# Kernel optimization log

Measured on AMD Instinct MI355X. Metric: run time of the kernel, lower is better.

## Reference

```python
import jax, jax.numpy as jnp
import numpy as np

BS, L, H, HD, R, HID = 4, 2048, 12, 64, 16, 768


def setup_inputs() -> dict:
    key = jax.random.key(0)
    k0, k1, k2, k3 = jax.random.split(key, 4)
    xavier = np.sqrt(2.0 / (H + HD))  # xavier_normal_ on (H, HD)
    lin = 1.0 / np.sqrt(HID)
    return {
        "hidden_states": jax.random.normal(k0, (BS, L, HID), jnp.float32),
        "K1_w": jax.random.normal(k1, (HID, H * HD), jnp.float32) * lin,
        "K1_b": jnp.zeros((H * HD,), jnp.float32),
        "V1_w": jax.random.normal(k2, (HID, H * HD), jnp.float32) * lin,
        "V1_b": jnp.zeros((H * HD,), jnp.float32),
        "ReadingHead": jax.random.normal(k3, (H, HD), jnp.float32) * xavier,
        "bidirection_weight": jnp.full((1, 1, H, 1, 2 * R), 1.0 / (2 * R), jnp.float32),
    }


def _scan_mmap(valid_mask, reverse):
    # valid_mask: (bs, L, H) bool. Sequential register-shift scan over positions 1..L-1.
    bs, Ln, Hn = valid_mask.shape
    idxs = jnp.arange(1, Ln, dtype=jnp.int32)
    masks = jnp.swapaxes(valid_mask[:, 1:], 0, 1)  # (L-1, bs, H)
    if reverse:
        idxs = idxs[::-1]
        masks = masks[::-1]
    init = jnp.zeros((bs, R + 1, Hn), jnp.int32)

    def step(valids, xm):
        i, m = xm
        valids = valids.at[:, 0].set(i)  # slot 0 <- current index (matches in-place torch order)
        shifted = jnp.where(m[:, None, :], valids[:, :-1], valids[:, 1:])
        valids = valids.at[:, 1:].set(shifted)
        return valids, valids[:, 1:]

    _, out = jax.lax.scan(step, init, (idxs, masks))  # (L-1, bs, R, H)
    if reverse:
        out = out[::-1]
    out = jnp.concatenate([jnp.zeros((1, bs, R, Hn), jnp.int32), out], axis=0)
    return jnp.swapaxes(out, 0, 1)  # (bs, L, R, H)


def reference(hidden_states, K1_w, K1_b, V1_w, V1_b, ReadingHead, bidirection_weight):
    K1 = jax.nn.relu(hidden_states @ K1_w + K1_b).reshape(BS, L, H, HD)
    V1 = jax.nn.relu(hidden_states @ V1_w + V1_b).reshape(BS, L, H, HD)
    dot_products = jnp.einsum('blhn,hn->blh', K1, ReadingHead)
    valid_mask = dot_products > 0.5  # attn_var default branch
    fm = _scan_mmap(valid_mask, False).reshape(BS, L * R, H)
    bm = _scan_mmap(valid_mask, True).reshape(BS, L * R, H)
    V_forward = jnp.take_along_axis(V1, fm[..., None], axis=1).reshape(BS, L, R, H, HD)
    V_backward = jnp.take_along_axis(V1, bm[..., None], axis=1).reshape(BS, L, R, H, HD)
    w = bidirection_weight[0, 0, :, 0, :]  # (H, 2R); first R -> forward, last R -> backward
    ctx = (jnp.einsum('blrhd,hr->blhd', V_forward, w[:, :R])
           + jnp.einsum('blrhd,hr->blhd', V_backward, w[:, R:]))
    return ctx.reshape(BS, L, H * HD)
```

## Files before the change

### kernel.cpp

```cpp
#include <hip/hip_runtime.h>
#include <hip/hip_bf16.h>

#define BS 4
#define L 2048
#define H 12
#define HD 64
#define R 16
#define HID 768
#define MARGIN 0.02f
#define FIXCAP 16384
#define FIXGRID 1024

typedef __attribute__((ext_vector_type(8))) short s8v;
typedef __attribute__((ext_vector_type(4))) float f32x4;

typedef __attribute__((address_space(1))) const void as1_void;
typedef __attribute__((address_space(3))) void as3_void;
#define GLOAD_LDS16(g, l) \
    __builtin_amdgcn_global_load_lds((as1_void*)(g), (as3_void*)(l), 16, 0, 0)

static __device__ __forceinline__ unsigned short f2bf_bits(float f) {
    __hip_bfloat16 h = __float2bfloat16(f);
    return *reinterpret_cast<unsigned short*>(&h);
}

__global__ __launch_bounds__(256) void convert_hs(
    const float* __restrict__ in, __hip_bfloat16* __restrict__ out,
    int* __restrict__ fixcnt)
{
    if (blockIdx.x == 0 && threadIdx.x == 0) *fixcnt = 0;
    int i = (blockIdx.x * 256 + threadIdx.x) * 4;
    float4 v = *(const float4*)&in[i];
    ushort4 o;
    o.x = f2bf_bits(v.x); o.y = f2bf_bits(v.y);
    o.z = f2bf_bits(v.z); o.w = f2bf_bits(v.w);
    *(ushort4*)&out[i] = o;
}

__global__ __launch_bounds__(256) void transpose_wt2(
    const float* __restrict__ K1w, const float* __restrict__ V1w,
    __hip_bfloat16* __restrict__ WtK, __hip_bfloat16* __restrict__ WtV)
{
    const float* in = blockIdx.z ? V1w : K1w;
    __hip_bfloat16* out = blockIdx.z ? WtV : WtK;
    __shared__ float s[32][33];
    const int c = threadIdx.x & 31, r8 = threadIdx.x >> 5;
    const int kt = blockIdx.x * 32, nt = blockIdx.y * 32;
#pragma unroll
    for (int rr = 0; rr < 4; ++rr) {
        int k = r8 + rr * 8;
        s[k][c] = in[(size_t)(kt + k) * HID + nt + c];
    }
    __syncthreads();
#pragma unroll
    for (int rr = 0; rr < 4; ++rr) {
        int n = r8 + rr * 8;
        out[(size_t)(nt + n) * HID + kt + c] = __float2bfloat16(s[c][n]);
    }
}

__global__ __launch_bounds__(256) void gemm_fused(
    const __hip_bfloat16* __restrict__ A,
    const __hip_bfloat16* __restrict__ WtK,
    const __hip_bfloat16* __restrict__ WtV,
    const float* __restrict__ K1b,
    const float* __restrict__ V1b,
    const float* __restrict__ RH,
    float* __restrict__ dots,
    int* __restrict__ fixlist,
    int* __restrict__ fixcnt,
    __hip_bfloat16* __restrict__ C)
{
    __shared__ alignas(16) __hip_bfloat16 As[128 * 64];
    __shared__ alignas(16) __hip_bfloat16 Bs[128 * 64];

    const int tid = threadIdx.x;
    const bool isV = blockIdx.y < 6;
    const int m0 = blockIdx.x * 128;
    const int n0 = (isV ? blockIdx.y : blockIdx.y - 6) * 128;
    const __hip_bfloat16* Bt = isV ? WtV : WtK;

    const int wid = tid >> 6, lane = tid & 63;
    const int quad = lane >> 4, lm = lane & 15;
    const int wm = wid & 1, wn = wid >> 1;

    const int srow = lane >> 3;
    const int schk = (lane & 7) ^ ((lane >> 3) & 7);
    const __hip_bfloat16* gA =
        A + (size_t)(m0 + 32 * wid + srow) * HID + schk * 8;
    const __hip_bfloat16* gB =
        Bt + (size_t)(n0 + 32 * wid + srow) * HID + schk * 8;
    __hip_bfloat16* lA = &As[(32 * wid) * 64];
    __hip_bfloat16* lB = &Bs[(32 * wid) * 64];

    const int s7 = lm & 7;
    const __hip_bfloat16* pA0 = &As[(wm * 64 + lm) * 64 + ((quad ^ s7) * 8)];
    const __hip_bfloat16* pA1 = &As[(wm * 64 + lm) * 64 + (((4 + quad) ^ s7) * 8)];
    const __hip_bfloat16* pB0 = &Bs[(wn * 64 + lm) * 64 + ((quad ^ s7) * 8)];
    const __hip_bfloat16* pB1 = &Bs[(wn * 64 + lm) * 64 + (((4 + quad) ^ s7) * 8)];

    f32x4 acc[4][4] = {};

    for (int k0 = 0; k0 < HID; k0 += 64) {
#pragma unroll
        for (int d = 0; d < 4; ++d) {
            GLOAD_LDS16(gA + (size_t)(8 * d) * HID, lA + (8 * d) * 64);
            GLOAD_LDS16(gB + (size_t)(8 * d) * HID, lB + (8 * d) * 64);
        }
        gA += 64; gB += 64;
        __syncthreads();

        s8v af[4], bf[4];
#pragma unroll
        for (int i = 0; i < 4; ++i) af[i] = *(const s8v*)(pA0 + i * 16 * 64);
#pragma unroll
        for (int j = 0; j < 4; ++j) bf[j] = *(const s8v*)(pB0 + j * 16 * 64);
#pragma unroll
        for (int i = 0; i < 4; ++i)
#pragma unroll
            for (int j = 0; j < 4; ++j)
                acc[i][j] = __builtin_amdgcn_mfma_f32_16x16x32_bf16(
                    af[i], bf[j], acc[i][j], 0, 0, 0);
#pragma unroll
        for (int i = 0; i < 4; ++i) af[i] = *(const s8v*)(pA1 + i * 16 * 64);
#pragma unroll
        for (int j = 0; j < 4; ++j) bf[j] = *(const s8v*)(pB1 + j * 16 * 64);
#pragma unroll
        for (int i = 0; i < 4; ++i)
#pragma unroll
            for (int j = 0; j < 4; ++j)
                acc[i][j] = __builtin_amdgcn_mfma_f32_16x16x32_bf16(
                    af[i], bf[j], acc[i][j], 0, 0, 0);
        __syncthreads();
    }

    if (isV) {
#pragma unroll
        for (int i = 0; i < 4; ++i) {
            int row_b = m0 + wm * 64 + i * 16 + quad * 4;
#pragma unroll
            for (int j = 0; j < 4; ++j) {
                int col = n0 + wn * 64 + j * 16 + lm;
                float bsv = V1b[col];
#pragma unroll
                for (int reg = 0; reg < 4; ++reg) {
                    float v = acc[i][j][reg] + bsv;
                    C[(size_t)(row_b + reg) * HID + col] =
                        __float2bfloat16(fmaxf(v, 0.f));
                }
            }
        }
    } else {
        const int head = (n0 >> 6) + wn;
        float bj[4], rj[4];
#pragma unroll
        for (int j = 0; j < 4; ++j) {
            bj[j] = K1b[head * 64 + j * 16 + lm];
            rj[j] = RH[head * 64 + j * 16 + lm];
        }
#pragma unroll
        for (int i = 0; i < 4; ++i) {
            int row0 = m0 + wm * 64 + i * 16 + quad * 4;
#pragma unroll
            for (int reg = 0; reg < 4; ++reg) {
                float p = 0.f;
#pragma unroll
                for (int j = 0; j < 4; ++j)
                    p = fmaf(fmaxf(acc[i][j][reg] + bj[j], 0.f), rj[j], p);
                p += __shfl_xor(p, 1, 64);
                p += __shfl_xor(p, 2, 64);
                p += __shfl_xor(p, 4, 64);
                p += __shfl_xor(p, 8, 64);
                if (lm == 0) {
                    int row = row0 + reg;
                    int b = row >> 11, l = row & (L - 1);
                    dots[((b * H + head) << 11) + l] = p;
                    if (fabsf(p - 0.5f) < MARGIN) {
                        int idx = atomicAdd(fixcnt, 1);
                        if (idx < FIXCAP) fixlist[idx] = row * 16 + head;
                    }
                }
            }
        }
    }
}

__global__ __launch_bounds__(256) void fixup_kernel(
    const float* __restrict__ hs,
    const float* __restrict__ W,
    const float* __restrict__ bias,
    const float* __restrict__ RH,
    const int* __restrict__ fixlist,
    const int* __restrict__ fixcnt,
    float* __restrict__ dots)
{
    __shared__ float hrow[HID];
    __shared__ float psum[4][64];

    const int tid = threadIdx.x;
    const int n = min(*fixcnt, FIXCAP);

    for (int item = blockIdx.x; item < n; item += FIXGRID) {
        int packed = fixlist[item];
        int row = packed >> 4, head = packed & 15;
        int b = row >> 11, l = row & (L - 1);

#pragma unroll
        for (int i = 0; i < 3; ++i)
            hrow[tid + i * 256] = hs[(size_t)row * HID + tid + i * 256];
        __syncthreads();

        const int d = tid & 63, kq = tid >> 6;
        float a0 = 0.f, a1 = 0.f;
#pragma unroll 8
        for (int i = 0; i < 96; ++i) {
            int k = kq + i * 8;
            a0 = fmaf(W[(size_t)k * HID + head * 64 + d], hrow[k], a0);
            a1 = fmaf(W[(size_t)(k + 4) * HID + head * 64 + d], hrow[k + 4], a1);
        }
        psum[kq][d] = a0 + a1;
        __syncthreads();
        if (tid < 64) {
            float v = psum[0][tid] + psum[1][tid] + psum[2][tid] +
                      psum[3][tid] + bias[head * 64 + tid];
            v = fmaxf(v, 0.f) * RH[head * 64 + tid];
#pragma unroll
            for (int s = 1; s < 64; s <<= 1) v += __shfl_xor(v, s, 64);
            if (tid == 0) dots[((size_t)(b * H + head) << 11) + l] = v;
        }
        __syncthreads();
    }
}

__global__ __launch_bounds__(256) void scan_kernel(
    const float* __restrict__ dots,
    unsigned short* __restrict__ Pg,
    unsigned short* __restrict__ Sg)
{
    __shared__ int wsum[4];
    const int bh = blockIdx.x;
    const int tid = threadIdx.x;
    const int base = tid * 8;
    const int lane = tid & 63, w = tid >> 6;

    int m[8], c[8];
    int run = 0;
#pragma unroll
    for (int i = 0; i < 8; ++i) {
        int l = base + i;
        m[i] = (l >= 1 && dots[((size_t)bh << 11) + l] > 0.5f) ? 1 : 0;
        run += m[i];
        c[i] = run;
    }
    int sc = run;
#pragma unroll
    for (int s = 1; s < 64; s <<= 1) {
        int v = __shfl_up(sc, s, 64);
        if (lane >= s) sc += v;
    }
    if (lane == 63) wsum[w] = sc;
    __syncthreads();
    int woff = 0;
    for (int i = 0; i < 4; ++i) if (i < w) woff += wsum[i];
    const int ex = woff + sc - run;

    union { unsigned short s[8]; uint4 q; } up;
#pragma unroll
    for (int i = 0; i < 8; ++i) {
        int pc = ex + c[i];
        up.s[i] = (unsigned short)pc;
        if (m[i]) Sg[((size_t)bh << 11) + pc] = (unsigned short)(base + i);
    }
    *(uint4*)&Pg[((size_t)bh << 11) + base] = up.q;
}

__global__ __launch_bounds__(256) void gather_kernel(
    const __hip_bfloat16* __restrict__ V1,
    const unsigned short* __restrict__ Pg,
    const unsigned short* __restrict__ Sg,
    const float* __restrict__ bw,
    float* __restrict__ out)
{
    __shared__ __hip_bfloat16 Vs[161 * 72];
    __shared__ unsigned short Ptile[129];
    __shared__ float sw[2 * R];
    __shared__ int sT;

    const int bh = blockIdx.y;
    const int b = bh / H, h = bh % H;
    const int l0 = blockIdx.x * 128;
    const int tid = threadIdx.x;

    if (tid < 129) {
        int l = l0 - 1 + tid;
        Ptile[tid] = (l >= 0) ? Pg[((size_t)bh << 11) + l] : (unsigned short)0;
    } else if (tid < 129 + 2 * R) {
        sw[tid - 129] = bw[h * (2 * R) + (tid - 129)];
    } else if (tid == 200) {
        sT = Pg[((size_t)bh << 11) + (L - 1)];
    }
    __syncthreads();

    const int T = sT;
    const int a = max(1, (int)Ptile[1] - (R - 1));
    const int bj = min(T, (int)Ptile[127] + R);
    const int nr = max(0, bj - a + 1);

    const __hip_bfloat16* Vbase = V1 + (size_t)b * L * HID + h * HD;
    for (int it = tid; it < (nr + 1) * 8; it += 256) {
        int slot = it >> 3, oct = it & 7;
        int row = slot ? (int)Sg[((size_t)bh << 11) + a + slot - 1] : 0;
        *(uint4*)&Vs[slot * 72 + oct * 8] =
            *(const uint4*)&Vbase[(size_t)row * HID + oct * 8];
    }
    __syncthreads();

    const int d8 = tid & 7, lg = tid >> 3;

#pragma unroll
    for (int li = 0; li < 4; ++li) {
        int ll = lg + 32 * li;
        int l = l0 + ll;
        int Pl = Ptile[1 + ll], Plm1 = Ptile[ll];
        bool lpos = (l >= 1);
        float acc0 = 0.f, acc1 = 0.f, acc2 = 0.f, acc3 = 0.f;
        float acc4 = 0.f, acc5 = 0.f, acc6 = 0.f, acc7 = 0.f;
#pragma unroll
        for (int r = 0; r < 2 * R; ++r) {
            int j, ok;
            if (r < R) { j = Pl - r;           ok = lpos && (j >= 1); }
            else       { j = Plm1 + 1 + (r - R); ok = lpos && (j <= T); }
            int slot = ok ? (j - a + 1) : 0;
            float wv = sw[r];
            uint4 uv = *(const uint4*)&Vs[slot * 72 + d8 * 8];
            acc0 = fmaf(wv, __uint_as_float(uv.x << 16), acc0);
            acc1 = fmaf(wv, __uint_as_float(uv.x & 0xffff0000u), acc1);
            acc2 = fmaf(wv, __uint_as_float(uv.y << 16), acc2);
            acc3 = fmaf(wv, __uint_as_float(uv.y & 0xffff0000u), acc3);
            acc4 = fmaf(wv, __uint_as_float(uv.z << 16), acc4);
            acc5 = fmaf(wv, __uint_as_float(uv.z & 0xffff0000u), acc5);
            acc6 = fmaf(wv, __uint_as_float(uv.w << 16), acc6);
            acc7 = fmaf(wv, __uint_as_float(uv.w & 0xffff0000u), acc7);
        }
        float* op = &out[((size_t)b * L + l) * HID + h * HD + d8 * 8];
        float4 o0, o1;
        o0.x = acc0; o0.y = acc1; o0.z = acc2; o0.w = acc3;
        o1.x = acc4; o1.y = acc5; o1.z = acc6; o1.w = acc7;
        *(float4*)op = o0;
        *(float4*)(op + 4) = o1;
    }
}

extern "C" void kernel_launch(void* const* d_in, const int* in_sizes, int n_in,
                              void* d_out, int out_size, void* d_ws, size_t ws_size,
                              hipStream_t stream) {
    const float* hs  = (const float*)d_in[0];
    const float* K1w = (const float*)d_in[1];
    const float* K1b = (const float*)d_in[2];
    const float* V1w = (const float*)d_in[3];
    const float* V1b = (const float*)d_in[4];
    const float* RH  = (const float*)d_in[5];
    const float* bw  = (const float*)d_in[6];
    float* out = (float*)d_out;

    __hip_bfloat16* Abf = (__hip_bfloat16*)d_out;

    char* ws = (char*)d_ws;
    __hip_bfloat16* WtV = (__hip_bfloat16*)ws;
    __hip_bfloat16* WtK = (__hip_bfloat16*)(ws + 1179648);
    __hip_bfloat16* V1  = (__hip_bfloat16*)(ws + 2359296);
    float* dots = (float*)(ws + 14942208);
    unsigned short* Pg = (unsigned short*)(ws + 15335424);
    unsigned short* Sg = (unsigned short*)(ws + 15532032);
    int* fixlist = (int*)(ws + 15728640);
    int* fixcnt  = (int*)(ws + 15794176);

    convert_hs<<<(BS * L * HID) / (256 * 4), 256, 0, stream>>>(hs, Abf, fixcnt);
    transpose_wt2<<<dim3(HID / 32, HID / 32, 2), 256, 0, stream>>>(K1w, V1w, WtK, WtV);
    gemm_fused<<<dim3(BS * L / 128, 12), 256, 0, stream>>>(
        Abf, WtK, WtV, K1b, V1b, RH, dots, fixlist, fixcnt, V1);
    fixup_kernel<<<FIXGRID, 256, 0, stream>>>(hs, K1w, K1b, RH, fixlist, fixcnt, dots);
    scan_kernel<<<BS * H, 256, 0, stream>>>(dots, Pg, Sg);
    gather_kernel<<<dim3(L / 128, BS * H), 256, 0, stream>>>(V1, Pg, Sg, bw, out);
}
```

Before: 170.1 us.

## Fuse hidden-state bf16 conversion into GEMM with register-prefetched K loop

Removes the separate convert_hs kernel and has the GEMM read fp32 hidden states directly, converting them to bf16 in registers before storing to LDS. The K loop now works on 32-wide slices with a register prefetch of the next tile in place of async global_load_lds, and the weight transpose absorbs the counter reset into a single prep kernel. This drops one launch and the bf16 round-trip through memory, but the GEMM reads the A operand as fp32 (twice the bytes) twelve times across the N blocks. It also syncs twice as often with a smaller K tile.

```diff
diff --git a/kernel.cpp b/kernel.cpp
--- a/kernel.cpp
+++ b/kernel.cpp
@@ -14,38 +14,24 @@
 typedef __attribute__((ext_vector_type(8))) short s8v;
 typedef __attribute__((ext_vector_type(4))) float f32x4;
 
-typedef __attribute__((address_space(1))) const void as1_void;
-typedef __attribute__((address_space(3))) void as3_void;
-#define GLOAD_LDS16(g, l) \
-    __builtin_amdgcn_global_load_lds((as1_void*)(g), (as3_void*)(l), 16, 0, 0)
-
 static __device__ __forceinline__ unsigned short f2bf_bits(float f) {
     __hip_bfloat16 h = __float2bfloat16(f);
     return *reinterpret_cast<unsigned short*>(&h);
 }
 
-__global__ __launch_bounds__(256) void convert_hs(
-    const float* __restrict__ in, __hip_bfloat16* __restrict__ out,
+__global__ __launch_bounds__(256) void prep_kernel(
+    const float* __restrict__ K1w, const float* __restrict__ V1w,
+    __hip_bfloat16* __restrict__ WtK, __hip_bfloat16* __restrict__ WtV,
     int* __restrict__ fixcnt)
 {
     if (blockIdx.x == 0 && threadIdx.x == 0) *fixcnt = 0;
-    int i = (blockIdx.x * 256 + threadIdx.x) * 4;
-    float4 v = *(const float4*)&in[i];
-    ushort4 o;
-    o.x = f2bf_bits(v.x); o.y = f2bf_bits(v.y);
-    o.z = f2bf_bits(v.z); o.w = f2bf_bits(v.w);
-    *(ushort4*)&out[i] = o;
-}
-
-__global__ __launch_bounds__(256) void transpose_wt2(
-    const float* __restrict__ K1w, const float* __restrict__ V1w,
-    __hip_bfloat16* __restrict__ WtK, __hip_bfloat16* __restrict__ WtV)
-{
-    const float* in = blockIdx.z ? V1w : K1w;
-    __hip_bfloat16* out = blockIdx.z ? WtV : WtK;
+    const int t = blockIdx.x;
+    const int z = t / 576, rem = t % 576;
+    const float* in = z ? V1w : K1w;
+    __hip_bfloat16* out = z ? WtV : WtK;
     __shared__ float s[32][33];
     const int c = threadIdx.x & 31, r8 = threadIdx.x >> 5;
-    const int kt = blockIdx.x * 32, nt = blockIdx.y * 32;
+    const int kt = (rem / 24) * 32, nt = (rem % 24) * 32;
 #pragma unroll
     for (int rr = 0; rr < 4; ++rr) {
         int k = r8 + rr * 8;
@@ -60,7 +46,7 @@
 }
 
 __global__ __launch_bounds__(256) void gemm_fused(
-    const __hip_bfloat16* __restrict__ A,
+    const float* __restrict__ A,
     const __hip_bfloat16* __restrict__ WtK,
     const __hip_bfloat16* __restrict__ WtV,
     const float* __restrict__ K1b,
@@ -71,8 +57,8 @@
     int* __restrict__ fixcnt,
     __hip_bfloat16* __restrict__ C)
 {
-    __shared__ alignas(16) __hip_bfloat16 As[128 * 64];
-    __shared__ alignas(16) __hip_bfloat16 Bs[128 * 64];
+    __shared__ alignas(16) __hip_bfloat16 As[128 * 32];
+    __shared__ alignas(16) __hip_bfloat16 Bs[128 * 32];
 
     const int tid = threadIdx.x;
     const bool isV = blockIdx.y < 6;
@@ -84,47 +70,57 @@
     const int quad = lane >> 4, lm = lane & 15;
     const int wm = wid & 1, wn = wid >> 1;
 
-    const int srow = lane >> 3;
-    const int schk = (lane & 7) ^ ((lane >> 3) & 7);
-    const __hip_bfloat16* gA =
-        A + (size_t)(m0 + 32 * wid + srow) * HID + schk * 8;
-    const __hip_bfloat16* gB =
-        Bt + (size_t)(n0 + 32 * wid + srow) * HID + schk * 8;
-    __hip_bfloat16* lA = &As[(32 * wid) * 64];
-    __hip_bfloat16* lB = &Bs[(32 * wid) * 64];
-
-    const int s7 = lm & 7;
-    const __hip_bfloat16* pA0 = &As[(wm * 64 + lm) * 64 + ((quad ^ s7) * 8)];
-    const __hip_bfloat16* pA1 = &As[(wm * 64 + lm) * 64 + (((4 + quad) ^ s7) * 8)];
-    const __hip_bfloat16* pB0 = &Bs[(wn * 64 + lm) * 64 + ((quad ^ s7) * 8)];
-    const __hip_bfloat16* pB1 = &Bs[(wn * 64 + lm) * 64 + (((4 + quad) ^ s7) * 8)];
+    const int r0 = tid >> 2,        c0 = tid & 3;
+    const int r1 = (tid + 256) >> 2, c1 = tid & 3;
+    const int p0 = c0 ^ ((r0 >> 1) & 3);
+    const int p1 = c1 ^ ((r1 >> 1) & 3);
+
+    const float* gA0 = A + (size_t)(m0 + r0) * HID + c0 * 8;
+    const float* gA1 = A + (size_t)(m0 + r1) * HID + c1 * 8;
+    const __hip_bfloat16* gB0 = Bt + (size_t)(n0 + r0) * HID + c0 * 8;
+    const __hip_bfloat16* gB1 = Bt + (size_t)(n0 + r1) * HID + c1 * 8;
+    uint4* wA0 = (uint4*)&As[r0 * 32 + p0 * 8];
+    uint4* wA1 = (uint4*)&As[r1 * 32 + p1 * 8];
+    uint4* wB0 = (uint4*)&Bs[r0 * 32 + p0 * 8];
+    uint4* wB1 = (uint4*)&Bs[r1 * 32 + p1 * 8];
+
+    const int fsw = (lm >> 1) & 3;
+    const __hip_bfloat16* pA = &As[(wm * 64 + lm) * 32 + ((quad ^ fsw) * 8)];
+    const __hip_bfloat16* pB = &Bs[(wn * 64 + lm) * 32 + ((quad ^ fsw) * 8)];
 
     f32x4 acc[4][4] = {};
 
-    for (int k0 = 0; k0 < HID; k0 += 64) {
-#pragma unroll
-        for (int d = 0; d < 4; ++d) {
-            GLOAD_LDS16(gA + (size_t)(8 * d) * HID, lA + (8 * d) * 64);
-            GLOAD_LDS16(gB + (size_t)(8 * d) * HID, lB + (8 * d) * 64);
-        }
-        gA += 64; gB += 64;
-        __syncthreads();
+    float4 a00 = *(const float4*)gA0, a01 = *(const float4*)(gA0 + 4);
+    float4 a10 = *(const float4*)gA1, a11 = *(const float4*)(gA1 + 4);
+    uint4  b0  = *(const uint4*)gB0,  b1  = *(const uint4*)gB1;
+    gA0 += 32; gA1 += 32; gB0 += 32; gB1 += 32;
+
+    for (int it = 0; it < HID / 32; ++it) {
+        union { unsigned short s[8]; uint4 v; } u0, u1;
+        u0.s[0] = f2bf_bits(a00.x); u0.s[1] = f2bf_bits(a00.y);
+        u0.s[2] = f2bf_bits(a00.z); u0.s[3] = f2bf_bits(a00.w);
+        u0.s[4] = f2bf_bits(a01.x); u0.s[5] = f2bf_bits(a01.y);
+        u0.s[6] = f2bf_bits(a01.z); u0.s[7] = f2bf_bits(a01.w);
+        u1.s[0] = f2bf_bits(a10.x); u1.s[1] = f2bf_bits(a10.y);
+        u1.s[2] = f2bf_bits(a10.z); u1.s[3] = f2bf_bits(a10.w);
+        u1.s[4] = f2bf_bits(a11.x); u1.s[5] = f2bf_bits(a11.y);
+        u1.s[6] = f2bf_bits(a11.z); u1.s[7] = f2bf_bits(a11.w);
+        *wA0 = u0.v; *wA1 = u1.v;
+        *wB0 = b0;   *wB1 = b1;
+        __syncthreads();
+
+        if (it + 1 < HID / 32) {
+            a00 = *(const float4*)gA0; a01 = *(const float4*)(gA0 + 4);
+            a10 = *(const float4*)gA1; a11 = *(const float4*)(gA1 + 4);
+            b0  = *(const uint4*)gB0;  b1  = *(const uint4*)gB1;
+            gA0 += 32; gA1 += 32; gB0 += 32; gB1 += 32;
+        }
 
         s8v af[4], bf[4];
 #pragma unroll
-        for (int i = 0; i < 4; ++i) af[i] = *(const s8v*)(pA0 + i * 16 * 64);
-#pragma unroll
-        for (int j = 0; j < 4; ++j) bf[j] = *(const s8v*)(pB0 + j * 16 * 64);
-#pragma unroll
-        for (int i = 0; i < 4; ++i)
-#pragma unroll
-            for (int j = 0; j < 4; ++j)
-                acc[i][j] = __builtin_amdgcn_mfma_f32_16x16x32_bf16(
-                    af[i], bf[j], acc[i][j], 0, 0, 0);
-#pragma unroll
-        for (int i = 0; i < 4; ++i) af[i] = *(const s8v*)(pA1 + i * 16 * 64);
-#pragma unroll
-        for (int j = 0; j < 4; ++j) bf[j] = *(const s8v*)(pB1 + j * 16 * 64);
+        for (int i = 0; i < 4; ++i) af[i] = *(const s8v*)(pA + i * 16 * 32);
+#pragma unroll
+        for (int j = 0; j < 4; ++j) bf[j] = *(const s8v*)(pB + j * 16 * 32);
 #pragma unroll
         for (int i = 0; i < 4; ++i)
 #pragma unroll
@@ -328,7 +324,7 @@
 #pragma unroll
         for (int r = 0; r < 2 * R; ++r) {
             int j, ok;
-            if (r < R) { j = Pl - r;           ok = lpos && (j >= 1); }
+            if (r < R) { j = Pl - r;             ok = lpos && (j >= 1); }
             else       { j = Plm1 + 1 + (r - R); ok = lpos && (j <= T); }
             int slot = ok ? (j - a + 1) : 0;
             float wv = sw[r];
@@ -363,8 +359,6 @@
     const float* bw  = (const float*)d_in[6];
     float* out = (float*)d_out;
 
-    __hip_bfloat16* Abf = (__hip_bfloat16*)d_out;
-
     char* ws = (char*)d_ws;
     __hip_bfloat16* WtV = (__hip_bfloat16*)ws;
     __hip_bfloat16* WtK = (__hip_bfloat16*)(ws + 1179648);
@@ -375,10 +369,9 @@
     int* fixlist = (int*)(ws + 15728640);
     int* fixcnt  = (int*)(ws + 15794176);
 
-    convert_hs<<<(BS * L * HID) / (256 * 4), 256, 0, stream>>>(hs, Abf, fixcnt);
-    transpose_wt2<<<dim3(HID / 32, HID / 32, 2), 256, 0, stream>>>(K1w, V1w, WtK, WtV);
+    prep_kernel<<<2 * 24 * 24, 256, 0, stream>>>(K1w, V1w, WtK, WtV, fixcnt);
     gemm_fused<<<dim3(BS * L / 128, 12), 256, 0, stream>>>(
-        Abf, WtK, WtV, K1b, V1b, RH, dots, fixlist, fixcnt, V1);
+        hs, WtK, WtV, K1b, V1b, RH, dots, fixlist, fixcnt, V1);
     fixup_kernel<<<FIXGRID, 256, 0, stream>>>(hs, K1w, K1b, RH, fixlist, fixcnt, dots);
     scan_kernel<<<BS * H, 256, 0, stream>>>(dots, Pg, Sg);
     gather_kernel<<<dim3(L / 128, BS * H), 256, 0, stream>>>(V1, Pg, Sg, bw, out);
```

Result: faster. 164.5 us (-3.2%).
